# Performance work log

Hardware: AMD Instinct MI355X
Metric: run time of the kernel (lower is better)

## Reference

```python
import jax, jax.numpy as jnp
import numpy as np
from functools import partial

T_TAGS = 14
START_IDX = 12
STOP_IDX = 13
HIDDEN = 1024        # hidden_dim
HD = HIDDEN // 2     # per-direction LSTM hidden
EMB = 768            # BERT embedding dim
SEQ = 8192           # number of steps (sentences)
NEG_INF = -10000.0


def _lstm_dir(x, w_ih, w_hh, b_ih, b_hh, h0, c0):
    # x: [S, EMB]; w_ih: [4*HD, EMB]; w_hh: [4*HD, HD]; torch gate order i,f,g,o
    xg = x @ w_ih.T + b_ih  # [S, 4*HD] precompute input projection

    def step(carry, xgt):
        h, c = carry
        g = xgt + h @ w_hh.T + b_hh
        i, f, gg, o = jnp.split(g, 4, axis=-1)
        c = jax.nn.sigmoid(f) * c + jax.nn.sigmoid(i) * jnp.tanh(gg)
        h = jax.nn.sigmoid(o) * jnp.tanh(c)
        return (h, c), h

    _, hs = jax.lax.scan(step, (h0, c0), xg)
    return hs  # [S, HD]


def _crf_forward(feats, transitions):
    # feats: [S, T]; transitions[j, i] = score of i -> j
    init = jnp.full((T_TAGS,), NEG_INF, dtype=feats.dtype).at[START_IDX].set(0.0)

    def step(fv, feat):
        # next[j] = logsumexp_i(fv[i] + trans[j,i]) + feat[j]
        nv = jax.nn.logsumexp(fv[None, :] + transitions, axis=1) + feat
        return nv, None

    fv, _ = jax.lax.scan(step, init, feats)
    return jax.nn.logsumexp(fv + transitions[STOP_IDX])


def _score_sentence(feats, tags, transitions):
    # tags: [S] int; prepend START
    tags_ext = jnp.concatenate([jnp.array([START_IDX], dtype=tags.dtype), tags])
    trans_score = transitions[tags_ext[1:], tags_ext[:-1]].sum()
    emit_score = feats[jnp.arange(feats.shape[0]), tags].sum()
    return trans_score + emit_score + transitions[STOP_IDX, tags[-1]]


def setup_inputs() -> dict:
    key = jax.random.key(0)
    ks = jax.random.split(key, 20)
    s_ih = 1.0 / np.sqrt(EMB)
    s_hh = 1.0 / np.sqrt(HD)

    embeds = jax.random.normal(ks[0], (SEQ, EMB), dtype=jnp.float32)
    tags = jax.random.randint(ks[1], (SEQ,), 0, 12)  # real tags only, no START/STOP

    w_ih_f = jax.random.normal(ks[2], (4 * HD, EMB), dtype=jnp.float32) * s_ih
    w_hh_f = jax.random.normal(ks[3], (4 * HD, HD), dtype=jnp.float32) * s_hh
    b_ih_f = jax.random.normal(ks[4], (4 * HD,), dtype=jnp.float32) * s_hh
    b_hh_f = jax.random.normal(ks[5], (4 * HD,), dtype=jnp.float32) * s_hh
    w_ih_b = jax.random.normal(ks[6], (4 * HD, EMB), dtype=jnp.float32) * s_ih
    w_hh_b = jax.random.normal(ks[7], (4 * HD, HD), dtype=jnp.float32) * s_hh
    b_ih_b = jax.random.normal(ks[8], (4 * HD,), dtype=jnp.float32) * s_hh
    b_hh_b = jax.random.normal(ks[9], (4 * HD,), dtype=jnp.float32) * s_hh

    w_tag = jax.random.normal(ks[10], (T_TAGS, HIDDEN), dtype=jnp.float32) / np.sqrt(HIDDEN)
    b_tag = jax.random.normal(ks[11], (T_TAGS,), dtype=jnp.float32) * 0.01

    transitions = jax.random.normal(ks[12], (T_TAGS, T_TAGS), dtype=jnp.float32)
    transitions = transitions.at[START_IDX, :].set(NEG_INF)
    transitions = transitions.at[:, STOP_IDX].set(NEG_INF)

    h0 = jax.random.normal(ks[13], (2, HD), dtype=jnp.float32)  # [dir, HD]
    c0 = jax.random.normal(ks[14], (2, HD), dtype=jnp.float32)

    return dict(embeds=embeds, tags=tags, w_ih_f=w_ih_f, w_hh_f=w_hh_f,
                b_ih_f=b_ih_f, b_hh_f=b_hh_f, w_ih_b=w_ih_b, w_hh_b=w_hh_b,
                b_ih_b=b_ih_b, b_hh_b=b_hh_b, w_tag=w_tag, b_tag=b_tag,
                transitions=transitions, h0=h0, c0=c0)


def reference(embeds, tags, w_ih_f, w_hh_f, b_ih_f, b_hh_f,
              w_ih_b, w_hh_b, b_ih_b, b_hh_b, w_tag, b_tag,
              transitions, h0, c0):
    # BiLSTM (dropout is identity in eval): forward dir + reversed backward dir
    hs_f = _lstm_dir(embeds, w_ih_f, w_hh_f, b_ih_f, b_hh_f, h0[0], c0[0])
    hs_b = _lstm_dir(embeds[::-1], w_ih_b, w_hh_b, b_ih_b, b_hh_b, h0[1], c0[1])[::-1]
    lstm_out = jnp.concatenate([hs_f, hs_b], axis=-1)  # [S, HIDDEN]
    feats = lstm_out @ w_tag.T + b_tag                  # [S, T_TAGS]

    forward_score = _crf_forward(feats, transitions)
    gold_score = _score_sentence(feats, tags, transitions)
    return forward_score - gold_score  # CRF negative log-likelihood (scalar)
```

## Files before the change

### kernel.cpp

```cpp
#include <hip/hip_runtime.h>
#include <hip/hip_bf16.h>

typedef unsigned int  uint32;
typedef unsigned short ushort16;
typedef float f32x2 __attribute__((ext_vector_type(2)));
typedef float f32x4 __attribute__((ext_vector_type(4)));
typedef short bf16x8 __attribute__((ext_vector_type(8)));

#define SEQN 8192
#define NBLK 32
#define UPB  16
#define K2E  1.4426950408889634f
#define LN2  0.6931471805599453f

#if __has_builtin(__builtin_amdgcn_exp2f)
#define EXP2F __builtin_amdgcn_exp2f
#else
#define EXP2F exp2f
#endif
#if __has_builtin(__builtin_amdgcn_logf)
#define LOG2F __builtin_amdgcn_logf
#else
#define LOG2F log2f
#endif
#if __has_builtin(__builtin_amdgcn_rcpf)
#define RCPF  __builtin_amdgcn_rcpf
#else
#define RCPF(x) (1.0f/(x))
#endif

__device__ __forceinline__ uint32 bf16_rne(float f) {
    uint32 u = __float_as_uint(f);
    return (u + 0x7fffu + ((u >> 16) & 1u)) >> 16;
}
__device__ __forceinline__ uint32 pack_bf16x2(float a, float b) {
    return bf16_rne(a) | (bf16_rne(b) << 16);
}
__device__ __forceinline__ float bfus(ushort16 u) { return __uint_as_float(((uint32)u) << 16); }
__device__ __forceinline__ float fsigmoid(float x) {
    return RCPF(1.f + EXP2F(-K2E * x));
}
__device__ __forceinline__ float ftanh_(float x) {
    float e = EXP2F(-2.f * K2E * fabsf(x));
    float r = (1.f - e) * RCPF(1.f + e);
    return copysignf(r, x);
}

__global__ __launch_bounds__(256) void convert_kernel(
    const float* __restrict__ embeds,
    const float* __restrict__ wihf, const float* __restrict__ wihb,
    const float* __restrict__ whhf, const float* __restrict__ whhb,
    uint32* __restrict__ emb16, uint32* __restrict__ wih16, uint32* __restrict__ whh16)
{
    int idx = blockIdx.x * 256 + threadIdx.x;
    if (idx < 3145728) {
        float2 v = ((const float2*)embeds)[idx];
        emb16[idx] = pack_bf16x2(v.x, v.y);
        return;
    }
    idx -= 3145728;
    if (idx < 1572864) {
        int d = idx / 786432;
        int p = idx - d * 786432;
        const float2* src = (const float2*)(d ? wihb : wihf);
        float2 v = src[p];
        wih16[idx] = pack_bf16x2(v.x, v.y);
        return;
    }
    idx -= 1572864;
    if (idx < 1048576) {
        int d    = idx >> 19;
        int rem  = idx & 524287;
        int blk  = rem >> 14;
        int s    = rem & 16383;
        int w    = s & 3;
        int q4   = s >> 2;
        int lane = q4 & 63;
        int i    = (q4 >> 6) & 15;
        int wv   = (q4 >> 10) & 3;
        int m    = lane & 15;
        int kq   = lane >> 4;
        int grow = wv * 512 + blk * 16 + m;
        int k0   = i * 32 + kq * 8 + 2 * w;
        const float* src = d ? whhb : whhf;
        whh16[idx] = pack_bf16x2(src[grow * 512 + k0], src[grow * 512 + k0 + 1]);
    }
}

__global__ __launch_bounds__(256) void gemm_xg_kernel(
    const ushort16* __restrict__ A,
    const ushort16* __restrict__ W,
    const float* __restrict__ bih, const float* __restrict__ bhh,
    ushort16* __restrict__ xgout,
    int reverse)
{
    const int lane = threadIdx.x & 63;
    const int wv = threadIdx.x >> 6;
    const int n_base = blockIdx.x * 64;
    const int m0 = blockIdx.y * 64 + wv * 16;
    const int lm = lane & 15;
    const int kq = lane >> 4;

    f32x4 acc[4];
    #pragma unroll
    for (int i = 0; i < 4; ++i) acc[i] = (f32x4){0.f, 0.f, 0.f, 0.f};

    int m = m0 + lm;
    int arow = reverse ? (SEQN - 1 - m) : m;
    const ushort16* aptr = A + (size_t)arow * 768 + kq * 8;
    const ushort16* wptr = W + kq * 8;

    for (int kk = 0; kk < 768; kk += 32) {
        bf16x8 af = *(const bf16x8*)(aptr + kk);
        #pragma unroll
        for (int nt = 0; nt < 4; ++nt) {
            int n = n_base + nt * 16 + lm;
            bf16x8 bfv = *(const bf16x8*)(wptr + (size_t)n * 768 + kk);
            acc[nt] = __builtin_amdgcn_mfma_f32_16x16x32_bf16(af, bfv, acc[nt], 0, 0, 0);
        }
    }
    const int mrow0 = m0 + kq * 4;
    #pragma unroll
    for (int nt = 0; nt < 4; ++nt) {
        int n = n_base + nt * 16 + lm;
        float bias = bih[n] + bhh[n];
        int blk2 = (n >> 4) & 31;
        int r    = ((n >> 9) << 4) | (n & 15);
        #pragma unroll
        for (int rg = 0; rg < 4; ++rg) {
            float v = acc[nt][rg] + bias;
            xgout[(size_t)(mrow0 + rg) * 2048 + blk2 * 64 + r] = (ushort16)bf16_rne(v);
        }
    }
}

__global__ __launch_bounds__(256) void lstm_scan_kernel(
    const uint4* __restrict__ whh_scan,
    const ushort16* __restrict__ xg,
    float* __restrict__ hs,
    const float* __restrict__ h0, const float* __restrict__ c0,
    uint32* __restrict__ xchg)
{
    __shared__ __align__(16) uint32 lds_h[256];
    __shared__ __align__(16) float lds_gates[64];

    const int tid = threadIdx.x;
    const int dir = blockIdx.x >> 5;
    const int blk = blockIdx.x & 31;
    const int wv = tid >> 6;
    const int lane = tid & 63;
    const int kq = lane >> 4;
    const bool bfl = (lane & 15) == 0;

    uint4 wreg[16];
    const uint4* wsl = whh_scan + (size_t)(dir * 32 + blk) * 4096 + (wv * 16) * 64 + lane;
    #pragma unroll
    for (int i = 0; i < 16; ++i) wreg[i] = wsl[i * 64];

    const ushort16* xg_d = xg + (size_t)dir * SEQN * 2048;
    float* hs_d = hs + (size_t)dir * SEQN * 512;
    uint32* xb = xchg + dir * 1024;

    float c = 0.f;
    if (tid < UPB) c = c0[dir * 512 + blk * UPB + tid];
    {
        float2 hv = *(const float2*)(h0 + dir * 512 + tid * 2);
        lds_h[tid] = pack_bf16x2(hv.x, hv.y);
    }
    __syncthreads();

    const uint4* lh4 = (const uint4*)lds_h;

    for (int t = 0; t < SEQN; ++t) {
        float xgv = 0.f;
        if (wv == 0) xgv = bfus(xg_d[(size_t)t * 2048 + blk * 64 + lane]);

        if (t > 0) {
            const uint32 tag = (uint32)t & 0xffffu;
            uint32* ps = xb + (((t - 1) & 1) << 9) + 2 * tid;
            uint32 a, b;
            for (;;) {
                a = __hip_atomic_load(ps,     __ATOMIC_RELAXED, __HIP_MEMORY_SCOPE_AGENT);
                b = __hip_atomic_load(ps + 1, __ATOMIC_RELAXED, __HIP_MEMORY_SCOPE_AGENT);
                if ((((a ^ tag) | (b ^ tag)) & 0xffffu) == 0u) break;
            }
            lds_h[tid] = (a >> 16) | (b & 0xffff0000u);
        }
        __syncthreads();

        f32x4 acc0 = (f32x4){0.f, 0.f, 0.f, 0.f};
        f32x4 acc1 = (f32x4){0.f, 0.f, 0.f, 0.f};
        #pragma unroll
        for (int i = 0; i < 16; i += 2) {
            uint4 h4a = (uint4){0, 0, 0, 0}, h4b = (uint4){0, 0, 0, 0};
            if (bfl) {
                h4a = lh4[i * 4 + kq];
                h4b = lh4[(i + 1) * 4 + kq];
            }
            acc0 = __builtin_amdgcn_mfma_f32_16x16x32_bf16(
                *(const bf16x8*)&wreg[i],     *(const bf16x8*)&h4a, acc0, 0, 0, 0);
            acc1 = __builtin_amdgcn_mfma_f32_16x16x32_bf16(
                *(const bf16x8*)&wreg[i + 1], *(const bf16x8*)&h4b, acc1, 0, 0, 0);
        }
        f32x4 s4 = acc0 + acc1;
        if (bfl) *(f32x4*)&lds_gates[wv * 16 + kq * 4] = s4;
        __syncthreads();

        if (wv == 0) {
            float gate = lds_gates[lane] + xgv;
            int u = lane & 15;
            float gi = __shfl(gate, u);
            float gf = __shfl(gate, 16 + u);
            float gg = __shfl(gate, 32 + u);
            float go = __shfl(gate, 48 + u);
            if (lane < UPB) {
                float iv = fsigmoid(gi), fvv = fsigmoid(gf);
                float gv = ftanh_(gg),   ov  = fsigmoid(go);
                c = fvv * c + iv * gv;
                float h = ov * ftanh_(c);
                int row_t = dir ? (SEQN - 1 - t) : t;
                hs_d[(size_t)row_t * 512 + blk * UPB + lane] = h;
                uint32 wd = (bf16_rne(h) << 16) | ((uint32)(t + 1) & 0xffffu);
                __hip_atomic_store(xb + ((t & 1) << 9) + blk * UPB + lane, wd,
                                   __ATOMIC_RELAXED, __HIP_MEMORY_SCOPE_AGENT);
            }
        }
    }
}

__global__ __launch_bounds__(256) void feats_kernel(
    const float* __restrict__ hsf, const float* __restrict__ hsb,
    const float* __restrict__ wtag, const float* __restrict__ btag,
    float* __restrict__ feats)
{
    __shared__ float4 lh[4096];
    int t0 = blockIdx.x * 16;
    for (int i = threadIdx.x; i < 4096; i += 256) {
        int row = i >> 8, c4 = i & 255;
        float4 v;
        if (c4 < 128) v = ((const float4*)hsf)[(size_t)(t0 + row) * 128 + c4];
        else          v = ((const float4*)hsb)[(size_t)(t0 + row) * 128 + (c4 - 128)];
        lh[i] = v;
    }
    __syncthreads();
    if (threadIdx.x < 224) {
        int r = threadIdx.x / 14;
        int j = threadIdx.x - r * 14;
        const float4* wr = (const float4*)wtag + j * 256;
        float acc = btag[j];
        #pragma unroll 8
        for (int kk = 0; kk < 256; ++kk) {
            float4 h = lh[r * 256 + kk];
            float4 w = wr[kk];
            acc += h.x * w.x + h.y * w.y + h.z * w.z + h.w * w.w;
        }
        feats[(size_t)(t0 + r) * 14 + j] = acc;
    }
}

__global__ __launch_bounds__(256) void gold_kernel(
    const int* __restrict__ tags, const float* __restrict__ trans,
    const float* __restrict__ feats, float* __restrict__ gold)
{
    __shared__ float red[256];
    float s = 0.f;
    for (int t = threadIdx.x; t < SEQN; t += 256) {
        int tg = tags[t];
        int pv = (t == 0) ? 12 : tags[t - 1];
        s += trans[tg * 14 + pv] + feats[(size_t)t * 14 + tg];
    }
    red[threadIdx.x] = s;
    __syncthreads();
    for (int st = 128; st > 0; st >>= 1) {
        if (threadIdx.x < st) red[threadIdx.x] += red[threadIdx.x + st];
        __syncthreads();
    }
    if (threadIdx.x == 0) gold[0] = red[0] + trans[13 * 14 + tags[SEQN - 1]];
}

__global__ __launch_bounds__(64) void crf_chunk_kernel(
    const float* __restrict__ feats, const float* __restrict__ trans,
    float* __restrict__ Mout)
{
    __shared__ float fl[1808];
    __shared__ float Mcol[256];
    const int c = blockIdx.x, l = threadIdx.x;
    for (int idx = l; idx < 1792; idx += 64) fl[idx] = feats[c * 1792 + idx] * K2E;
    if (l < 16) fl[1792 + l] = 0.f;
    const int i = l >> 2, q = l & 3;
    const bool act = (i < 14);
    float T2[4][14];
    #pragma unroll
    for (int jj = 0; jj < 4; ++jj) {
        int j = q + 4 * jj;
        #pragma unroll
        for (int k = 0; k < 14; ++k)
            T2[jj][k] = (act && j < 14) ? trans[j * 14 + k] * K2E : -30000.f;
    }
    __syncthreads();

    float nv[4];
    #pragma unroll
    for (int jj = 0; jj < 4; ++jj) {
        int j = q + 4 * jj;
        nv[jj] = (act && j < 14) ? (T2[jj][i] + fl[j]) : -30000.f;
    }

    for (int t = 1; t < 128; ++t) {
        if (act) {
            #pragma unroll
            for (int jj = 0; jj < 4; ++jj) {
                int j = q + 4 * jj;
                if (j < 14) Mcol[i * 16 + j] = nv[jj];
            }
        }
        __syncthreads();
        float Mc[16];
        *(f32x4*)&Mc[0]  = *(const f32x4*)&Mcol[i * 16];
        *(f32x4*)&Mc[4]  = *(const f32x4*)&Mcol[i * 16 + 4];
        *(f32x4*)&Mc[8]  = *(const f32x4*)&Mcol[i * 16 + 8];
        *(f32x4*)&Mc[12] = *(const f32x4*)&Mcol[i * 16 + 12];
        #pragma unroll
        for (int jj = 0; jj < 4; ++jj) {
            int j = q + 4 * jj;
            float x[14];
            #pragma unroll
            for (int k = 0; k < 14; ++k) x[k] = T2[jj][k] + Mc[k];
            float m01 = fmaxf(x[0], x[1]),  m23 = fmaxf(x[2], x[3]);
            float m45 = fmaxf(x[4], x[5]),  m67 = fmaxf(x[6], x[7]);
            float m89 = fmaxf(x[8], x[9]),  mab = fmaxf(x[10], x[11]);
            float mcd = fmaxf(x[12], x[13]);
            float m = fmaxf(fmaxf(fmaxf(m01, m23), fmaxf(m45, m67)),
                            fmaxf(fmaxf(m89, mab), mcd));
            float s = 0.f;
            #pragma unroll
            for (int k = 0; k < 14; ++k) s += EXP2F(x[k] - m);
            nv[jj] = m + LOG2F(s) + fl[t * 14 + j];
        }
        __syncthreads();
    }
    if (act) {
        #pragma unroll
        for (int jj = 0; jj < 4; ++jj) {
            int j = q + 4 * jj;
            if (j < 14) Mout[c * 224 + j * 16 + i] = nv[jj];
        }
    }
}

__global__ __launch_bounds__(64) void crf_combine_kernel(
    const float* __restrict__ M, const float* __restrict__ trans,
    const float* __restrict__ gold, float* __restrict__ out)
{
    const int j = threadIdx.x;
    const int jc = (j < 14) ? j : 0;
    float V[14];
    #pragma unroll
    for (int i = 0; i < 14; ++i) V[i] = (i == 12) ? 0.f : -10000.f * K2E;
    for (int cc = 0; cc < 64; ++cc) {
        const float* Mr = M + cc * 224 + jc * 16;
        float4 r0 = *(const float4*)(Mr);
        float4 r1 = *(const float4*)(Mr + 4);
        float4 r2 = *(const float4*)(Mr + 8);
        float4 r3 = *(const float4*)(Mr + 12);
        float x[14] = {r0.x + V[0], r0.y + V[1], r0.z + V[2],  r0.w + V[3],
                       r1.x + V[4], r1.y + V[5], r1.z + V[6],  r1.w + V[7],
                       r2.x + V[8], r2.y + V[9], r2.z + V[10], r2.w + V[11],
                       r3.x + V[12], r3.y + V[13]};
        float m = x[0];
        #pragma unroll
        for (int k = 1; k < 14; ++k) m = fmaxf(m, x[k]);
        float s = 0.f;
        #pragma unroll
        for (int k = 0; k < 14; ++k) s += EXP2F(x[k] - m);
        float nv = m + LOG2F(s);
        #pragma unroll
        for (int i = 0; i < 14; ++i) V[i] = __shfl(nv, i);
    }
    if (j == 0) {
        float x[14];
        #pragma unroll
        for (int i = 0; i < 14; ++i) x[i] = V[i] + trans[13 * 14 + i] * K2E;
        float m = x[0];
        #pragma unroll
        for (int k = 1; k < 14; ++k) m = fmaxf(m, x[k]);
        float s = 0.f;
        #pragma unroll
        for (int k = 0; k < 14; ++k) s += EXP2F(x[k] - m);
        out[0] = LN2 * (m + LOG2F(s)) - gold[0];
    }
}

extern "C" void kernel_launch(void* const* d_in, const int* in_sizes, int n_in,
                              void* d_out, int out_size, void* d_ws, size_t ws_size,
                              hipStream_t stream) {
    const float* embeds = (const float*)d_in[0];
    const int*   tags   = (const int*)d_in[1];
    const float* wihf   = (const float*)d_in[2];
    const float* whhf   = (const float*)d_in[3];
    const float* bihf   = (const float*)d_in[4];
    const float* bhhf   = (const float*)d_in[5];
    const float* wihb   = (const float*)d_in[6];
    const float* whhb   = (const float*)d_in[7];
    const float* bihb   = (const float*)d_in[8];
    const float* bhhb   = (const float*)d_in[9];
    const float* wtag   = (const float*)d_in[10];
    const float* btag   = (const float*)d_in[11];
    const float* trans  = (const float*)d_in[12];
    const float* h0     = (const float*)d_in[13];
    const float* c0     = (const float*)d_in[14];

    char* ws = (char*)d_ws;
    uint32*   emb16 = (uint32*)(ws);
    uint32*   wih16 = (uint32*)(ws + 12582912);
    uint32*   whh16 = (uint32*)(ws + 18874368);
    ushort16* xg    = (ushort16*)(ws + 23068672);
    float*    hs    = (float*)(ws + 90177536);
    float*    feats = (float*)(ws + 123731968);
    uint32*   xchg  = (uint32*)(ws + 124190720);
    float*    crfM  = (float*)(ws + 124198912);
    float*    gold  = (float*)(ws + 124256256);

    convert_kernel<<<22528, 256, 0, stream>>>(embeds, wihf, wihb, whhf, whhb,
                                              emb16, wih16, whh16);
    gemm_xg_kernel<<<dim3(32, 128), 256, 0, stream>>>(
        (const ushort16*)emb16, (const ushort16*)wih16, bihf, bhhf, xg, 0);
    gemm_xg_kernel<<<dim3(32, 128), 256, 0, stream>>>(
        (const ushort16*)emb16, (const ushort16*)(wih16 + 786432), bihb, bhhb,
        xg + (size_t)SEQN * 2048, 1);
    lstm_scan_kernel<<<64, 256, 0, stream>>>((const uint4*)whh16, xg, hs, h0, c0, xchg);
    feats_kernel<<<512, 256, 0, stream>>>(hs, hs + (size_t)SEQN * 512, wtag, btag, feats);
    gold_kernel<<<1, 256, 0, stream>>>(tags, trans, feats, gold);
    crf_chunk_kernel<<<64, 64, 0, stream>>>(feats, trans, crfM);
    crf_combine_kernel<<<1, 64, 0, stream>>>(crfM, trans, gold, (float*)d_out);
}
```

Before: 13.84 ms.

## Reorganize LSTM scan so each wave computes all four gates for its units

The recurrent weights and the precomputed input gates are reordered so that each MFMA output column holds the i, f, g and o gates of one hidden unit. Every wave can then apply the LSTM cell update directly, which removes the LDS gate buffer, the second barrier's reduction step and the shuffles through wave 0. Input-gate values are prefetched into LDS in double-buffered chunks of 16 timesteps rather than loaded from global memory on every step. The polling loop reads both exchange words with one 64-bit atomic load, and the h vector is loaded into registers before the MFMA chain. In exchange the kernel uses more registers and LDS, and the prefetch store depends on the barrier ordering staying correct.

```diff
diff --git a/kernel.cpp b/kernel.cpp
--- a/kernel.cpp
+++ b/kernel.cpp
@@ -9,7 +9,6 @@
 
 #define SEQN 8192
 #define NBLK 32
-#define UPB  16
 #define K2E  1.4426950408889634f
 #define LN2  0.6931471805599453f
 
@@ -36,7 +35,8 @@
 __device__ __forceinline__ uint32 pack_bf16x2(float a, float b) {
     return bf16_rne(a) | (bf16_rne(b) << 16);
 }
-__device__ __forceinline__ float bfus(ushort16 u) { return __uint_as_float(((uint32)u) << 16); }
+__device__ __forceinline__ float bflo(uint32 u) { return __uint_as_float(u << 16); }
+__device__ __forceinline__ float bfhi(uint32 u) { return __uint_as_float(u & 0xffff0000u); }
 __device__ __forceinline__ float fsigmoid(float x) {
     return RCPF(1.f + EXP2F(-K2E * x));
 }
@@ -69,20 +69,19 @@
     }
     idx -= 1572864;
     if (idx < 1048576) {
-        int d    = idx >> 19;
-        int rem  = idx & 524287;
-        int blk  = rem >> 14;
-        int s    = rem & 16383;
-        int w    = s & 3;
-        int q4   = s >> 2;
-        int lane = q4 & 63;
-        int i    = (q4 >> 6) & 15;
-        int wv   = (q4 >> 10) & 3;
-        int m    = lane & 15;
-        int kq   = lane >> 4;
-        int grow = wv * 512 + blk * 16 + m;
-        int k0   = i * 32 + kq * 8 + 2 * w;
-        const float* src = d ? whhb : whhf;
+        int d    = idx & 3;
+        int l    = (idx >> 2) & 63;
+        int i    = (idx >> 8) & 15;
+        int w    = (idx >> 12) & 3;
+        int blk  = (idx >> 14) & 31;
+        int dir  = (idx >> 19) & 1;
+        int m    = l & 15;
+        int kq   = l >> 4;
+        int up   = m >> 2;
+        int g    = m & 3;
+        int grow = g * 512 + blk * 16 + w * 4 + up;
+        int k0   = i * 32 + kq * 8 + 2 * d;
+        const float* src = dir ? whhb : whhf;
         whh16[idx] = pack_bf16x2(src[grow * 512 + k0], src[grow * 512 + k0 + 1]);
     }
 }
@@ -124,12 +123,13 @@
     for (int nt = 0; nt < 4; ++nt) {
         int n = n_base + nt * 16 + lm;
         float bias = bih[n] + bhh[n];
-        int blk2 = (n >> 4) & 31;
-        int r    = ((n >> 9) << 4) | (n & 15);
+        int g  = n >> 9;
+        int ug = n & 511;
+        int oidx = (ug >> 4) * 64 + (ug & 15) * 4 + g;
         #pragma unroll
         for (int rg = 0; rg < 4; ++rg) {
             float v = acc[nt][rg] + bias;
-            xgout[(size_t)(mrow0 + rg) * 2048 + blk2 * 64 + r] = (ushort16)bf16_rne(v);
+            xgout[(size_t)(mrow0 + rg) * 2048 + oidx] = (ushort16)bf16_rne(v);
         }
     }
 }
@@ -142,7 +142,7 @@
     uint32* __restrict__ xchg)
 {
     __shared__ __align__(16) uint32 lds_h[256];
-    __shared__ __align__(16) float lds_gates[64];
+    __shared__ __align__(16) uint32 lds_xg[1024];
 
     const int tid = threadIdx.x;
     const int dir = blockIdx.x >> 5;
@@ -150,80 +150,88 @@
     const int wv = tid >> 6;
     const int lane = tid & 63;
     const int kq = lane >> 4;
-    const bool bfl = (lane & 15) == 0;
+    const bool act = (lane & 15) == 0;
+    const int u_loc = wv * 4 + kq;
 
     uint4 wreg[16];
-    const uint4* wsl = whh_scan + (size_t)(dir * 32 + blk) * 4096 + (wv * 16) * 64 + lane;
-    #pragma unroll
-    for (int i = 0; i < 16; ++i) wreg[i] = wsl[i * 64];
+    {
+        const uint4* wsl = whh_scan + (size_t)((dir * 32 + blk) * 4 + wv) * 1024 + lane;
+        #pragma unroll
+        for (int i = 0; i < 16; ++i) wreg[i] = wsl[i * 64];
+    }
 
     const ushort16* xg_d = xg + (size_t)dir * SEQN * 2048;
     float* hs_d = hs + (size_t)dir * SEQN * 512;
     uint32* xb = xchg + dir * 1024;
 
     float c = 0.f;
-    if (tid < UPB) c = c0[dir * 512 + blk * UPB + tid];
+    if (act) c = c0[dir * 512 + blk * 16 + u_loc];
+
     {
         float2 hv = *(const float2*)(h0 + dir * 512 + tid * 2);
         lds_h[tid] = pack_bf16x2(hv.x, hv.y);
     }
+    {
+        int s = tid >> 4, p = tid & 15;
+        uint2 v = *(const uint2*)(xg_d + (size_t)s * 2048 + blk * 64 + p * 4);
+        *(uint2*)&lds_xg[s * 32 + p * 2] = v;
+    }
     __syncthreads();
 
     const uint4* lh4 = (const uint4*)lds_h;
 
     for (int t = 0; t < SEQN; ++t) {
-        float xgv = 0.f;
-        if (wv == 0) xgv = bfus(xg_d[(size_t)t * 2048 + blk * 64 + lane]);
-
         if (t > 0) {
-            const uint32 tag = (uint32)t & 0xffffu;
-            uint32* ps = xb + (((t - 1) & 1) << 9) + 2 * tid;
-            uint32 a, b;
-            for (;;) {
-                a = __hip_atomic_load(ps,     __ATOMIC_RELAXED, __HIP_MEMORY_SCOPE_AGENT);
-                b = __hip_atomic_load(ps + 1, __ATOMIC_RELAXED, __HIP_MEMORY_SCOPE_AGENT);
-                if ((((a ^ tag) | (b ^ tag)) & 0xffffu) == 0u) break;
-            }
-            lds_h[tid] = (a >> 16) | (b & 0xffff0000u);
+            const unsigned long long tagpat =
+                ((unsigned long long)(uint32)t << 32) | (uint32)t;
+            const unsigned long long* ps =
+                (const unsigned long long*)(xb + (((t - 1) & 1) << 9)) + tid;
+            unsigned long long v;
+            do {
+                v = __hip_atomic_load(ps, __ATOMIC_RELAXED, __HIP_MEMORY_SCOPE_AGENT);
+            } while (((v ^ tagpat) & 0x0000ffff0000ffffull) != 0ull);
+            lds_h[tid] = ((uint32)(v >> 16) & 0xffffu) | ((uint32)(v >> 32) & 0xffff0000u);
         }
         __syncthreads();
 
-        f32x4 acc0 = (f32x4){0.f, 0.f, 0.f, 0.f};
-        f32x4 acc1 = (f32x4){0.f, 0.f, 0.f, 0.f};
-        #pragma unroll
-        for (int i = 0; i < 16; i += 2) {
-            uint4 h4a = (uint4){0, 0, 0, 0}, h4b = (uint4){0, 0, 0, 0};
-            if (bfl) {
-                h4a = lh4[i * 4 + kq];
-                h4b = lh4[(i + 1) * 4 + kq];
-            }
-            acc0 = __builtin_amdgcn_mfma_f32_16x16x32_bf16(
-                *(const bf16x8*)&wreg[i],     *(const bf16x8*)&h4a, acc0, 0, 0, 0);
-            acc1 = __builtin_amdgcn_mfma_f32_16x16x32_bf16(
-                *(const bf16x8*)&wreg[i + 1], *(const bf16x8*)&h4b, acc1, 0, 0, 0);
-        }
-        f32x4 s4 = acc0 + acc1;
-        if (bfl) *(f32x4*)&lds_gates[wv * 16 + kq * 4] = s4;
+        if ((t & 15) == 0 && t + 16 < SEQN) {
+            int s = tid >> 4, p = tid & 15;
+            uint2 v = *(const uint2*)(xg_d + (size_t)(t + 16 + s) * 2048 + blk * 64 + p * 4);
+            int buf = ((t >> 4) + 1) & 1;
+            *(uint2*)&lds_xg[buf * 512 + s * 32 + p * 2] = v;
+        }
+
+        uint4 hreg[16];
+        #pragma unroll
+        for (int i = 0; i < 16; ++i) hreg[i] = lh4[i * 4 + kq];
         __syncthreads();
 
-        if (wv == 0) {
-            float gate = lds_gates[lane] + xgv;
-            int u = lane & 15;
-            float gi = __shfl(gate, u);
-            float gf = __shfl(gate, 16 + u);
-            float gg = __shfl(gate, 32 + u);
-            float go = __shfl(gate, 48 + u);
-            if (lane < UPB) {
-                float iv = fsigmoid(gi), fvv = fsigmoid(gf);
-                float gv = ftanh_(gg),   ov  = fsigmoid(go);
-                c = fvv * c + iv * gv;
-                float h = ov * ftanh_(c);
-                int row_t = dir ? (SEQN - 1 - t) : t;
-                hs_d[(size_t)row_t * 512 + blk * UPB + lane] = h;
-                uint32 wd = (bf16_rne(h) << 16) | ((uint32)(t + 1) & 0xffffu);
-                __hip_atomic_store(xb + ((t & 1) << 9) + blk * UPB + lane, wd,
-                                   __ATOMIC_RELAXED, __HIP_MEMORY_SCOPE_AGENT);
-            }
+        f32x4 a0 = (f32x4){0.f,0.f,0.f,0.f}, a1 = (f32x4){0.f,0.f,0.f,0.f};
+        f32x4 a2 = (f32x4){0.f,0.f,0.f,0.f}, a3 = (f32x4){0.f,0.f,0.f,0.f};
+        #pragma unroll
+        for (int i = 0; i < 4; ++i) {
+            a0 = __builtin_amdgcn_mfma_f32_16x16x32_bf16(*(const bf16x8*)&wreg[i],      *(const bf16x8*)&hreg[i],      a0, 0, 0, 0);
+            a1 = __builtin_amdgcn_mfma_f32_16x16x32_bf16(*(const bf16x8*)&wreg[4 + i],  *(const bf16x8*)&hreg[4 + i],  a1, 0, 0, 0);
+            a2 = __builtin_amdgcn_mfma_f32_16x16x32_bf16(*(const bf16x8*)&wreg[8 + i],  *(const bf16x8*)&hreg[8 + i],  a2, 0, 0, 0);
+            a3 = __builtin_amdgcn_mfma_f32_16x16x32_bf16(*(const bf16x8*)&wreg[12 + i], *(const bf16x8*)&hreg[12 + i], a3, 0, 0, 0);
+        }
+        f32x4 s4 = (a0 + a1) + (a2 + a3);
+
+        if (act) {
+            uint2 xv = *(const uint2*)&lds_xg[((t >> 4) & 1) * 512 + (t & 15) * 32 + u_loc * 2];
+            float gi = s4[0] + bflo(xv.x);
+            float gf = s4[1] + bfhi(xv.x);
+            float gg = s4[2] + bflo(xv.y);
+            float go = s4[3] + bfhi(xv.y);
+            float iv = fsigmoid(gi), fvv = fsigmoid(gf);
+            float gv = ftanh_(gg),   ov  = fsigmoid(go);
+            c = fvv * c + iv * gv;
+            float h = ov * ftanh_(c);
+            int row_t = dir ? (SEQN - 1 - t) : t;
+            hs_d[(size_t)row_t * 512 + blk * 16 + u_loc] = h;
+            uint32 wd = (bf16_rne(h) << 16) | ((uint32)(t + 1) & 0xffffu);
+            __hip_atomic_store(xb + ((t & 1) << 9) + blk * 16 + u_loc, wd,
+                               __ATOMIC_RELAXED, __HIP_MEMORY_SCOPE_AGENT);
         }
     }
 }
```

After: 14.43 ms. 1.04x slower.
